# Performance work log

Measured on AMD Instinct MI355X. Metric: run time of the kernel, lower is better.

The kernel has to match this reference:

```python
import jax, jax.numpy as jnp
import numpy as np

H, C = 3, 64          # heads, out_channels
NEG_SLOPE = 0.2       # PyG GATConv leaky_relu default
LN_EPS = 1e-5


def setup_inputs() -> dict:
    key = jax.random.key(0)
    ks = jax.random.split(key, 20)
    N, E, D_in, edge_dim = 50000, 800000, 64, 5
    g = lambda k, shape: (jax.random.normal(k, shape, dtype=jnp.float32) * 0.1)
    return {
        "x": jax.random.normal(ks[0], (N, D_in), dtype=jnp.float32),
        "edge_attr": jax.random.normal(ks[1], (E, edge_dim), dtype=jnp.float32),
        "lin_w": g(ks[2], (D_in, H * C)),          # GATConv.lin (bias=False)
        "att_src": g(ks[3], (H, C)),
        "att_dst": g(ks[4], (H, C)),
        "lin_edge_w": g(ks[5], (edge_dim, H * C)),  # GATConv.lin_edge (bias=False)
        "att_edge": g(ks[6], (H, C)),
        "gat_bias": jnp.zeros((H * C,), jnp.float32),
        "w1": g(ks[7], (H * C, C)),
        "b1": jnp.zeros((C,), jnp.float32),
        "ln1_g": jnp.ones((C,), jnp.float32),
        "ln1_b": jnp.zeros((C,), jnp.float32),
        "w2": g(ks[8], (C, C)),
        "b2": jnp.zeros((C,), jnp.float32),
        "ln2_g": jnp.ones((C,), jnp.float32),
        "ln2_b": jnp.zeros((C,), jnp.float32),
        "edge_index": jax.random.randint(ks[9], (2, E), 0, N),
    }


def layer_norm(x, g, b):
    m = jnp.mean(x, axis=-1, keepdims=True)
    v = jnp.mean((x - m) ** 2, axis=-1, keepdims=True)
    return (x - m) * jax.lax.rsqrt(v + LN_EPS) * g + b


def gat_conv(x, edge_index, edge_attr, lin_w, att_src, att_dst,
             lin_edge_w, att_edge, gat_bias):
    N = x.shape[0]
    src, dst = edge_index[0], edge_index[1]

    # add_self_loops=True with fill_value='mean': self-loop edge_attr is the
    # per-node mean of incoming edge attributes (0 if node has no in-edges).
    attr_sum = jax.ops.segment_sum(edge_attr, dst, num_segments=N)       # [N, edge_dim]
    cnt = jax.ops.segment_sum(jnp.ones((dst.shape[0],), edge_attr.dtype), dst, num_segments=N)
    loop_attr = attr_sum / jnp.maximum(cnt, 1.0)[:, None]
    loop = jnp.arange(N, dtype=src.dtype)
    src = jnp.concatenate([src, loop])
    dst = jnp.concatenate([dst, loop])
    ea = jnp.concatenate([edge_attr, loop_attr], axis=0)                  # [E2, edge_dim]

    xs = (x @ lin_w).reshape(N, H, C)                                     # [N, H, C]
    a_src = jnp.einsum('nhc,hc->nh', xs, att_src)                         # [N, H]
    a_dst = jnp.einsum('nhc,hc->nh', xs, att_dst)                         # [N, H]
    e = (ea @ lin_edge_w).reshape(-1, H, C)                               # [E2, H, C]
    a_edge = jnp.einsum('ehc,hc->eh', e, att_edge)                        # [E2, H]

    logits = a_src[src] + a_dst[dst] + a_edge                             # [E2, H]
    logits = jnp.where(logits >= 0, logits, NEG_SLOPE * logits)           # leaky_relu

    # segment softmax over incoming edges of each dst node (self loops ensure non-empty)
    lmax = jax.ops.segment_max(logits, dst, num_segments=N)               # [N, H]
    ex = jnp.exp(logits - lmax[dst])
    denom = jax.ops.segment_sum(ex, dst, num_segments=N)                  # [N, H]
    alpha = ex / denom[dst]                                               # [E2, H]

    msgs = alpha[:, :, None] * xs[src]                                    # [E2, H, C]
    out = jax.ops.segment_sum(msgs, dst, num_segments=N)                  # [N, H, C]
    return out.reshape(N, H * C) + gat_bias


def reference(x, edge_attr, lin_w, att_src, att_dst, lin_edge_w, att_edge,
              gat_bias, w1, b1, ln1_g, ln1_b, w2, b2, ln2_g, ln2_b, edge_index):
    x_gat = gat_conv(x, edge_index, edge_attr, lin_w, att_src, att_dst,
                     lin_edge_w, att_edge, gat_bias)
    x_gat = x_gat @ w1 + b1                         # linear1: [N, C]
    x_gat = layer_norm(x + x_gat, ln1_g, ln1_b)     # layerNorm1(x + x_gat)
    lin = x_gat @ w2 + b2                           # linear2
    out = layer_norm(lin + x_gat, ln2_g, ln2_b)     # layerNorm2(lin + x_gat)
    return out                                      # dropout p=0 -> identity
```

## Files before the change

### kernel.cpp

```cpp
#include <hip/hip_runtime.h>


#define HH 3
#define CC 64
#define DIN 64
#define ED 5
#define HC 192
#define NEG_SLOPE 0.2f
#define LN_EPS 1e-5f
#define LOG2E 1.44269504f

typedef __attribute__((ext_vector_type(8))) short bf16x8;
typedef __attribute__((ext_vector_type(4))) float f32x4;

__device__ __forceinline__ float leaky(float l) { return fmaxf(l, NEG_SLOPE * l); }

__device__ __forceinline__ unsigned short f2bf(float f) {
    unsigned u = __float_as_uint(f);
    unsigned r = (u + 0x7FFFu + ((u >> 16) & 1u)) >> 16;
    return (unsigned short)r;
}
__device__ __forceinline__ float bf2f(unsigned short u) {
    return __uint_as_float((unsigned)u << 16);
}
__device__ __forceinline__ float bf_lo(unsigned v) { return __uint_as_float(v << 16); }
__device__ __forceinline__ float bf_hi(unsigned v) { return __uint_as_float(v & 0xFFFF0000u); }
__device__ __forceinline__ float rdl_f(float v, int i) {
    return __int_as_float(__builtin_amdgcn_readlane(__float_as_int(v), i));
}

__device__ __forceinline__ bf16x8 pack8(float4 a, float4 b) {
    bf16x8 r;
    r[0] = (short)f2bf(a.x); r[1] = (short)f2bf(a.y);
    r[2] = (short)f2bf(a.z); r[3] = (short)f2bf(a.w);
    r[4] = (short)f2bf(b.x); r[5] = (short)f2bf(b.y);
    r[6] = (short)f2bf(b.z); r[7] = (short)f2bf(b.w);
    return r;
}

#define PREP_TOT (HC*DIN + DIN*HC + CC*CC + CC + ED*HH)
#define PREP_BLOCKS 30
__global__ __launch_bounds__(256) void k_prep_cnt(const float* __restrict__ lin_w,
                                                  const float* __restrict__ w1,
                                                  const float* __restrict__ w2,
                                                  const float* __restrict__ b1,
                                                  const float* __restrict__ gat_bias,
                                                  const float* __restrict__ lin_edge_w,
                                                  const float* __restrict__ att_edge,
                                                  unsigned short* __restrict__ linwt,
                                                  unsigned short* __restrict__ w1t,
                                                  unsigned short* __restrict__ w2t,
                                                  float* __restrict__ b1p,
                                                  float* __restrict__ we,
                                                  const int* __restrict__ ei,
                                                  int* __restrict__ icnt, int E) {
    if (blockIdx.x < PREP_BLOCKS) {
        for (int i = blockIdx.x * 256 + threadIdx.x; i < PREP_TOT; i += PREP_BLOCKS * 256) {
            if (i < HC * DIN) {
                int c = i >> 6, k = i & 63;
                linwt[i] = f2bf(lin_w[k * HC + c]);
            } else if (i < 2 * HC * DIN) {
                int j = i - HC * DIN;
                int c = j / HC, k = j - c * HC;
                w1t[j] = f2bf(w1[k * CC + c]);
            } else if (i < 2 * HC * DIN + CC * CC) {
                int j = i - 2 * HC * DIN;
                int c = j >> 6, k = j & 63;
                w2t[j] = f2bf(w2[k * CC + c]);
            } else if (i < 2 * HC * DIN + CC * CC + CC) {
                int c = i - (2 * HC * DIN + CC * CC);
                float s = b1[c];
                for (int k = 0; k < HC; ++k) s += gat_bias[k] * w1[k * CC + c];
                b1p[c] = s;
            } else {
                int q = i - (2 * HC * DIN + CC * CC + CC);
                int d = q / HH, h = q - d * HH;
                float s = 0.f;
                for (int c = 0; c < CC; ++c)
                    s += lin_edge_w[d * HC + h * CC + c] * att_edge[h * CC + c];
                we[q] = s * LOG2E;
            }
        }
    } else {
        int nb = gridDim.x - PREP_BLOCKS;
        for (int e = (blockIdx.x - PREP_BLOCKS) * 256 + threadIdx.x; e < E; e += nb * 256)
            atomicAdd(&icnt[ei[E + e]], 1);
    }
}

__global__ __launch_bounds__(256) void k_xs(const float* __restrict__ x,
                                            const unsigned short* __restrict__ linwt,
                                            const float* __restrict__ att_src,
                                            const float* __restrict__ att_dst,
                                            unsigned short* __restrict__ xsb,
                                            float* __restrict__ a_src,
                                            float* __restrict__ a_dst, int N) {
    int lane = threadIdx.x & 63, w = threadIdx.x >> 6;
    int l15 = lane & 15, kg = (lane >> 4) * 8;
    int nb = blockIdx.x * 64;
    int arow = nb + w * 16 + l15;
    int arow_c = min(arow, N - 1);

    f32x4 acc[12];
    #pragma unroll
    for (int ct = 0; ct < 12; ++ct) acc[ct] = (f32x4){0.f, 0.f, 0.f, 0.f};

    #pragma unroll
    for (int k0 = 0; k0 < DIN; k0 += 32) {
        const float* ap = x + (size_t)arow_c * DIN + k0 + kg;
        float4 a0 = *(const float4*)ap;
        float4 a1 = *(const float4*)(ap + 4);
        bf16x8 af = pack8(a0, a1);
        #pragma unroll
        for (int ct = 0; ct < 12; ++ct) {
            bf16x8 bf = *(const bf16x8*)(linwt + (size_t)(ct * 16 + l15) * DIN + k0 + kg);
            acc[ct] = __builtin_amdgcn_mfma_f32_16x16x32_bf16(af, bf, acc[ct], 0, 0, 0);
        }
    }

    float asv[12], adv[12];
    #pragma unroll
    for (int ct = 0; ct < 12; ++ct) {
        int c = ct * 16 + l15;
        asv[ct] = att_src[c]; adv[ct] = att_dst[c];
    }

    int rbase = nb + w * 16 + (lane >> 4) * 4;
    #pragma unroll
    for (int j = 0; j < 4; ++j) {
        int r = rbase + j;
        bool ok = r < N;
        float ps0 = 0.f, ps1 = 0.f, ps2 = 0.f, pd0 = 0.f, pd1 = 0.f, pd2 = 0.f;
        #pragma unroll
        for (int ct = 0; ct < 12; ++ct) {
            float v = acc[ct][j];
            float s = v * asv[ct], d = v * adv[ct];
            if (ct < 4)      { ps0 += s; pd0 += d; }
            else if (ct < 8) { ps1 += s; pd1 += d; }
            else             { ps2 += s; pd2 += d; }
        }
        if (ok) {
            unsigned* row32 = (unsigned*)(xsb + (size_t)r * HC);
            #pragma unroll
            for (int ct = 0; ct < 4; ++ct) {
                int c = ct * 16 + l15;
                row32[c] = (unsigned)f2bf(acc[ct][j]) | ((unsigned)f2bf(acc[ct + 4][j]) << 16);
                xsb[(size_t)r * HC + 128 + c] = f2bf(acc[ct + 8][j]);
            }
        }
        #pragma unroll
        for (int o = 1; o < 16; o <<= 1) {
            ps0 += __shfl_xor(ps0, o, 64); pd0 += __shfl_xor(pd0, o, 64);
            ps1 += __shfl_xor(ps1, o, 64); pd1 += __shfl_xor(pd1, o, 64);
            ps2 += __shfl_xor(ps2, o, 64); pd2 += __shfl_xor(pd2, o, 64);
        }
        if (ok && l15 == 0) {
            a_src[r * HH + 0] = ps0 * LOG2E; a_src[r * HH + 1] = ps1 * LOG2E;
            a_src[r * HH + 2] = ps2 * LOG2E;
            a_dst[r * HH + 0] = pd0 * LOG2E; a_dst[r * HH + 1] = pd1 * LOG2E;
            a_dst[r * HH + 2] = pd2 * LOG2E;
        }
    }
}

__global__ __launch_bounds__(256) void k_scanA(const int* __restrict__ icnt,
                                               int* __restrict__ gtot,
                                               int* __restrict__ off,
                                               int* __restrict__ cursor, int N) {
    int i = blockIdx.x * 256 + threadIdx.x;
    int lane = threadIdx.x & 63, wid = threadIdx.x >> 6;
    int v = (i < N) ? icnt[i] : 0;
    int incl = v;
    #pragma unroll
    for (int o = 1; o < 64; o <<= 1) {
        int u = __shfl_up(incl, o, 64);
        if (lane >= o) incl += u;
    }
    __shared__ int wt[4];
    __shared__ int base_sh;
    if (lane == 63) wt[wid] = incl;
    __syncthreads();
    if (threadIdx.x == 0)
        base_sh = atomicAdd(gtot, wt[0] + wt[1] + wt[2] + wt[3]);
    __syncthreads();
    int wpre = 0;
    for (int w = 0; w < wid; ++w) wpre += wt[w];
    int excl = base_sh + wpre + incl - v;
    if (i < N) {
        off[i] = excl;
        cursor[i] = excl;
    }
}

__global__ __launch_bounds__(256) void k_fill(const float* __restrict__ ea,
                                              const int* __restrict__ ei,
                                              const float* __restrict__ a_src,
                                              const float* __restrict__ a_dst,
                                              const float* __restrict__ we,
                                              int* __restrict__ cursor,
                                              uint4* __restrict__ payload, int E) {
    int e = blockIdx.x * blockDim.x + threadIdx.x;
    if (e >= E) return;
    int s = ei[e], d = ei[E + e];
    float attr[ED];
    #pragma unroll
    for (int j = 0; j < ED; ++j) attr[j] = ea[(size_t)e * ED + j];
    float aeh[HH], lp[HH];
    #pragma unroll
    for (int h = 0; h < HH; ++h) {
        float a = 0.f;
        #pragma unroll
        for (int j = 0; j < ED; ++j) a += attr[j] * we[j * HH + h];
        aeh[h] = a;
        lp[h] = a_src[s * HH + h] + a_dst[d * HH + h] + a;
    }
    int pos = atomicAdd(&cursor[d], 1);
    uint4 pk;
    pk.x = (unsigned)f2bf(lp[0])  | ((unsigned)f2bf(lp[1])  << 16);
    pk.y = (unsigned)f2bf(lp[2])  | ((unsigned)f2bf(aeh[0]) << 16);
    pk.z = (unsigned)f2bf(aeh[1]) | ((unsigned)f2bf(aeh[2]) << 16);
    pk.w = (unsigned)s;
    payload[pos] = pk;
}

__global__ __launch_bounds__(256) void k_gat(const unsigned short* __restrict__ xsb,
                                             const float* __restrict__ a_src,
                                             const float* __restrict__ a_dst,
                                             const int* __restrict__ off,
                                             const int* __restrict__ icnt,
                                             const uint4* __restrict__ payload,
                                             unsigned short* __restrict__ oaccb, int N) {
    int lane = threadIdx.x & 63;
    int wid  = threadIdx.x >> 6;
    const unsigned* xs32 = (const unsigned*)xsb;
    unsigned c128ml = 128u - (unsigned)lane;
    for (int n = blockIdx.x * 4 + wid; n < N; n += gridDim.x * 4) {
        int beg = off[n];
        int deg = icnt[n];

        float pden0 = 0.f, pden1 = 0.f, pden2 = 0.f;
        float pae0 = 0.f, pae1 = 0.f, pae2 = 0.f;
        float a0A = 0.f, a1A = 0.f, a2A = 0.f;
        float a0B = 0.f, a1B = 0.f, a2B = 0.f;

        for (int c0 = 0; c0 < deg; c0 += 64) {
            int cn = min(deg - c0, 64);
            float w0 = 0.f, w1 = 0.f, w2 = 0.f;
            int srcv = 0;
            if (lane < cn) {
                uint4 p = payload[beg + c0 + lane];
                w0 = exp2f(leaky(bf_lo(p.x)));
                w1 = exp2f(leaky(bf_hi(p.x)));
                w2 = exp2f(leaky(bf_lo(p.y)));
                pae0 += bf_hi(p.y);
                pae1 += bf_lo(p.z);
                pae2 += bf_hi(p.z);
                pden0 += w0; pden1 += w1; pden2 += w2;
                srcv = (int)p.w;
            }
            int i = 0;
            for (; i + 2 <= cn; i += 2) {
                float ta0 = rdl_f(w0, i),     ta1 = rdl_f(w1, i),     ta2 = rdl_f(w2, i);
                int   sa  = __builtin_amdgcn_readlane(srcv, i);
                float tb0 = rdl_f(w0, i + 1), tb1 = rdl_f(w1, i + 1), tb2 = rdl_f(w2, i + 1);
                int   sb  = __builtin_amdgcn_readlane(srcv, i + 1);
                unsigned ia = (unsigned)sa * 96u + lane;
                unsigned ib = (unsigned)sb * 96u + lane;
                unsigned va = xs32[ia];
                unsigned vb = xs32[ib];
                float xa2 = bf2f(xsb[(ia << 1) + c128ml]);
                float xb2 = bf2f(xsb[(ib << 1) + c128ml]);
                a0A += ta0 * bf_lo(va); a1A += ta1 * bf_hi(va); a2A += ta2 * xa2;
                a0B += tb0 * bf_lo(vb); a1B += tb1 * bf_hi(vb); a2B += tb2 * xb2;
            }
            if (i < cn) {
                float ta0 = rdl_f(w0, i), ta1 = rdl_f(w1, i), ta2 = rdl_f(w2, i);
                int   sa  = __builtin_amdgcn_readlane(srcv, i);
                unsigned ia = (unsigned)sa * 96u + lane;
                unsigned va = xs32[ia];
                a0A += ta0 * bf_lo(va);
                a1A += ta1 * bf_hi(va);
                a2A += ta2 * bf2f(xsb[(ia << 1) + c128ml]);
            }
        }

        #pragma unroll
        for (int o = 32; o; o >>= 1) {
            pden0 += __shfl_xor(pden0, o, 64);
            pden1 += __shfl_xor(pden1, o, 64);
            pden2 += __shfl_xor(pden2, o, 64);
            pae0  += __shfl_xor(pae0, o, 64);
            pae1  += __shfl_xor(pae1, o, 64);
            pae2  += __shfl_xor(pae2, o, 64);
        }

        float dc = fmaxf((float)deg, 1.0f);
        float inv_dc = __builtin_amdgcn_rcpf(dc);
        float sl0 = leaky(a_src[n * HH + 0] + a_dst[n * HH + 0] + pae0 * inv_dc);
        float sl1 = leaky(a_src[n * HH + 1] + a_dst[n * HH + 1] + pae1 * inv_dc);
        float sl2 = leaky(a_src[n * HH + 2] + a_dst[n * HH + 2] + pae2 * inv_dc);
        float e0 = exp2f(sl0), e1 = exp2f(sl1), e2 = exp2f(sl2);
        unsigned ian = (unsigned)n * 96u + lane;
        unsigned van = xs32[ian];
        float xn2 = bf2f(xsb[(ian << 1) + c128ml]);
        float r0 = __builtin_amdgcn_rcpf(pden0 + e0);
        float r1 = __builtin_amdgcn_rcpf(pden1 + e1);
        float r2 = __builtin_amdgcn_rcpf(pden2 + e2);
        float acc0 = (a0A + a0B + e0 * bf_lo(van)) * r0;
        float acc1 = (a1A + a1B + e1 * bf_hi(van)) * r1;
        float acc2 = (a2A + a2B + e2 * xn2) * r2;
        size_t nbse = (size_t)n * HC;
        oaccb[nbse + 0 * CC + lane] = f2bf(acc0);
        oaccb[nbse + 1 * CC + lane] = f2bf(acc1);
        oaccb[nbse + 2 * CC + lane] = f2bf(acc2);
    }
}

__global__ __launch_bounds__(256) void k_mlp(const unsigned short* __restrict__ oaccb,
                                             const unsigned short* __restrict__ w1t,
                                             const unsigned short* __restrict__ w2t,
                                             const float* __restrict__ b1p,
                                             const float* __restrict__ x,
                                             const float* __restrict__ g1,
                                             const float* __restrict__ be1,
                                             const float* __restrict__ b2,
                                             const float* __restrict__ g2,
                                             const float* __restrict__ be2,
                                             float* __restrict__ out, int N) {
    __shared__ unsigned short H1[64 * 72];
    int lane = threadIdx.x & 63, w = threadIdx.x >> 6;
    int l15 = lane & 15, kg = (lane >> 4) * 8;
    int nb = blockIdx.x * 64;
    int arow = nb + w * 16 + l15;
    int arow_c = min(arow, N - 1);

    float c_b1[4], c_g1[4], c_be1[4], c_b2[4], c_g2[4], c_be2[4];
    #pragma unroll
    for (int ct = 0; ct < 4; ++ct) {
        int c = ct * 16 + l15;
        c_b1[ct] = b1p[c]; c_g1[ct] = g1[c]; c_be1[ct] = be1[c];
        c_b2[ct] = b2[c];  c_g2[ct] = g2[c]; c_be2[ct] = be2[c];
    }

    f32x4 acc[4];
    #pragma unroll
    for (int ct = 0; ct < 4; ++ct) acc[ct] = (f32x4){0.f, 0.f, 0.f, 0.f};
    #pragma unroll
    for (int k0 = 0; k0 < HC; k0 += 32) {
        bf16x8 af = *(const bf16x8*)(oaccb + (size_t)arow_c * HC + k0 + kg);
        #pragma unroll
        for (int ct = 0; ct < 4; ++ct) {
            bf16x8 bf = *(const bf16x8*)(w1t + (size_t)(ct * 16 + l15) * HC + k0 + kg);
            acc[ct] = __builtin_amdgcn_mfma_f32_16x16x32_bf16(af, bf, acc[ct], 0, 0, 0);
        }
    }

    int rbase = nb + w * 16 + (lane >> 4) * 4;
    int rloc0 = w * 16 + (lane >> 4) * 4;
    float h1v[4][4];
    float y[4][4];
    #pragma unroll
    for (int j = 0; j < 4; ++j) {
        int r = min(rbase + j, N - 1);
        #pragma unroll
        for (int ct = 0; ct < 4; ++ct)
            y[ct][j] = acc[ct][j] + c_b1[ct] + x[(size_t)r * DIN + ct * 16 + l15];
    }
    #pragma unroll
    for (int j = 0; j < 4; ++j) {
        float s = y[0][j] + y[1][j] + y[2][j] + y[3][j];
        #pragma unroll
        for (int o = 1; o < 16; o <<= 1) s += __shfl_xor(s, o, 64);
        float m = s * (1.0f / CC);
        float vs = 0.f;
        #pragma unroll
        for (int ct = 0; ct < 4; ++ct) { float d = y[ct][j] - m; vs += d * d; }
        #pragma unroll
        for (int o = 1; o < 16; o <<= 1) vs += __shfl_xor(vs, o, 64);
        float inv = rsqrtf(vs * (1.0f / CC) + LN_EPS);
        #pragma unroll
        for (int ct = 0; ct < 4; ++ct) {
            float h = (y[ct][j] - m) * inv * c_g1[ct] + c_be1[ct];
            h1v[ct][j] = h;
            H1[(rloc0 + j) * 72 + ct * 16 + l15] = f2bf(h);
        }
    }
    __syncthreads();

    f32x4 acc2[4];
    #pragma unroll
    for (int ct = 0; ct < 4; ++ct) acc2[ct] = (f32x4){0.f, 0.f, 0.f, 0.f};
    #pragma unroll
    for (int k0 = 0; k0 < CC; k0 += 32) {
        bf16x8 af = *(const bf16x8*)&H1[(w * 16 + l15) * 72 + k0 + kg];
        #pragma unroll
        for (int ct = 0; ct < 4; ++ct) {
            bf16x8 bf = *(const bf16x8*)(w2t + (size_t)(ct * 16 + l15) * CC + k0 + kg);
            acc2[ct] = __builtin_amdgcn_mfma_f32_16x16x32_bf16(af, bf, acc2[ct], 0, 0, 0);
        }
    }

    #pragma unroll
    for (int j = 0; j < 4; ++j) {
        float z0 = acc2[0][j] + c_b2[0] + h1v[0][j];
        float z1 = acc2[1][j] + c_b2[1] + h1v[1][j];
        float z2 = acc2[2][j] + c_b2[2] + h1v[2][j];
        float z3 = acc2[3][j] + c_b2[3] + h1v[3][j];
        float s = z0 + z1 + z2 + z3;
        #pragma unroll
        for (int o = 1; o < 16; o <<= 1) s += __shfl_xor(s, o, 64);
        float m = s * (1.0f / CC);
        float d0 = z0 - m, d1 = z1 - m, d2 = z2 - m, d3 = z3 - m;
        float vs = d0 * d0 + d1 * d1 + d2 * d2 + d3 * d3;
        #pragma unroll
        for (int o = 1; o < 16; o <<= 1) vs += __shfl_xor(vs, o, 64);
        float inv = rsqrtf(vs * (1.0f / CC) + LN_EPS);
        int r = rbase + j;
        if (r < N) {
            out[(size_t)r * CC + 0 * 16 + l15] = d0 * inv * c_g2[0] + c_be2[0];
            out[(size_t)r * CC + 1 * 16 + l15] = d1 * inv * c_g2[1] + c_be2[1];
            out[(size_t)r * CC + 2 * 16 + l15] = d2 * inv * c_g2[2] + c_be2[2];
            out[(size_t)r * CC + 3 * 16 + l15] = d3 * inv * c_g2[3] + c_be2[3];
        }
    }
}

extern "C" void kernel_launch(void* const* d_in, const int* in_sizes, int n_in,
                              void* d_out, int out_size, void* d_ws, size_t ws_size,
                              hipStream_t stream) {
    const float* x          = (const float*)d_in[0];
    const float* edge_attr  = (const float*)d_in[1];
    const float* lin_w      = (const float*)d_in[2];
    const float* att_src    = (const float*)d_in[3];
    const float* att_dst    = (const float*)d_in[4];
    const float* lin_edge_w = (const float*)d_in[5];
    const float* att_edge   = (const float*)d_in[6];
    const float* gat_bias   = (const float*)d_in[7];
    const float* w1         = (const float*)d_in[8];
    const float* b1         = (const float*)d_in[9];
    const float* ln1_g      = (const float*)d_in[10];
    const float* ln1_b      = (const float*)d_in[11];
    const float* w2         = (const float*)d_in[12];
    const float* b2         = (const float*)d_in[13];
    const float* ln2_g      = (const float*)d_in[14];
    const float* ln2_b      = (const float*)d_in[15];
    const int*   ei         = (const int*)d_in[16];
    float* out = (float*)d_out;

    const int N = in_sizes[0] / DIN;
    const int E = in_sizes[1] / ED;
    const int nb_scan = (N + 255) / 256;

    char* ws = (char*)d_ws;
    size_t off_b = 0;
    auto alloc = [&](size_t bytes) {
        size_t o = off_b;
        off_b = (off_b + bytes + 255) & ~(size_t)255;
        return o;
    };
    int* icnt = (int*)(ws + alloc((size_t)N * 4));
    int* gtot = (int*)(ws + alloc(4));
    size_t zero_bytes = off_b;
    unsigned short* xsb   = (unsigned short*)(ws + alloc((size_t)N * HC * 2));
    unsigned short* oaccb = (unsigned short*)(ws + alloc((size_t)N * HC * 2));
    float*  a_srcb  = (float*)(ws + alloc((size_t)N * HH * 4));
    float*  a_dstb  = (float*)(ws + alloc((size_t)N * HH * 4));
    int*    offb    = (int*)(ws + alloc((size_t)N * 4));
    int*    cursor  = (int*)(ws + alloc((size_t)N * 4));
    uint4*  payload = (uint4*)(ws + alloc((size_t)E * 16));
    unsigned short* linwt = (unsigned short*)(ws + alloc((size_t)HC * DIN * 2));
    unsigned short* w1t   = (unsigned short*)(ws + alloc((size_t)DIN * HC * 2));
    unsigned short* w2t   = (unsigned short*)(ws + alloc((size_t)CC * CC * 2));
    float* b1p = (float*)(ws + alloc((size_t)CC * 4));
    float* we  = (float*)(ws + alloc((size_t)ED * HH * 4));
    (void)ws_size; (void)n_in; (void)out_size;

    hipMemsetAsync(d_ws, 0, zero_bytes, stream);

    k_prep_cnt<<<PREP_BLOCKS + (E + 255) / 256, 256, 0, stream>>>(
        lin_w, w1, w2, b1, gat_bias, lin_edge_w, att_edge,
        linwt, w1t, w2t, b1p, we, ei, icnt, E);
    k_xs<<<(N + 63) / 64, 256, 0, stream>>>(x, linwt, att_src, att_dst, xsb, a_srcb, a_dstb, N);
    k_scanA<<<nb_scan, 256, 0, stream>>>(icnt, gtot, offb, cursor, N);
    k_fill<<<(E + 255) / 256, 256, 0, stream>>>(edge_attr, ei, a_srcb, a_dstb, we, cursor,
                                                payload, E);
    k_gat<<<(N + 3) / 4, 256, 0, stream>>>(xsb, a_srcb, a_dstb, offb, icnt, payload, oaccb, N);
    k_mlp<<<(N + 63) / 64, 256, 0, stream>>>(oaccb, w1t, w2t, b1p, x,
                                             ln1_g, ln1_b, b2, ln2_g, ln2_b, out, N);
}
```

Baseline: 186.9 us.

## Merge scan into xs kernel, stage edge weights in LDS, hoist fill atomic

The block-level scan of in-degree counts now runs as extra blocks of the xs projection kernel, which removes one kernel launch. In the gather kernel, per-edge weights and source indices are written to a per-wave LDS buffer and read back as float4 instead of being broadcast with readlane. The fill kernel issues its cursor atomic earlier so its latency can overlap the attribute loads, and the index multiplies use __umul24. These are several unrelated tweaks, and the LDS staging adds shared-memory traffic where readlane had none.

New measurement: 184.9 us. Within noise of the previous version (-1.0%).

```diff
diff --git a/kernel.cpp b/kernel.cpp
--- a/kernel.cpp
+++ b/kernel.cpp
@@ -25,9 +25,6 @@
 }
 __device__ __forceinline__ float bf_lo(unsigned v) { return __uint_as_float(v << 16); }
 __device__ __forceinline__ float bf_hi(unsigned v) { return __uint_as_float(v & 0xFFFF0000u); }
-__device__ __forceinline__ float rdl_f(float v, int i) {
-    return __int_as_float(__builtin_amdgcn_readlane(__float_as_int(v), i));
-}
 
 __device__ __forceinline__ bf16x8 pack8(float4 a, float4 b) {
     bf16x8 r;
@@ -94,7 +91,37 @@
                                             const float* __restrict__ att_dst,
                                             unsigned short* __restrict__ xsb,
                                             float* __restrict__ a_src,
-                                            float* __restrict__ a_dst, int N) {
+                                            float* __restrict__ a_dst,
+                                            const int* __restrict__ icnt,
+                                            int* __restrict__ gtot,
+                                            int* __restrict__ off,
+                                            int* __restrict__ cursor,
+                                            int N, int nbx) {
+    __shared__ int wt[4];
+    __shared__ int base_sh;
+    if ((int)blockIdx.x >= nbx) {
+        int bid = blockIdx.x - nbx;
+        int i = bid * 256 + threadIdx.x;
+        int lane = threadIdx.x & 63, wid = threadIdx.x >> 6;
+        int v = (i < N) ? icnt[i] : 0;
+        int incl = v;
+        #pragma unroll
+        for (int o = 1; o < 64; o <<= 1) {
+            int u = __shfl_up(incl, o, 64);
+            if (lane >= o) incl += u;
+        }
+        if (lane == 63) wt[wid] = incl;
+        __syncthreads();
+        if (threadIdx.x == 0)
+            base_sh = atomicAdd(gtot, wt[0] + wt[1] + wt[2] + wt[3]);
+        __syncthreads();
+        int wpre = 0;
+        for (int w2 = 0; w2 < wid; ++w2) wpre += wt[w2];
+        int excl = base_sh + wpre + incl - v;
+        if (i < N) { off[i] = excl; cursor[i] = excl; }
+        return;
+    }
+
     int lane = threadIdx.x & 63, w = threadIdx.x >> 6;
     int l15 = lane & 15, kg = (lane >> 4) * 8;
     int nb = blockIdx.x * 64;
@@ -160,35 +187,6 @@
             a_dst[r * HH + 0] = pd0 * LOG2E; a_dst[r * HH + 1] = pd1 * LOG2E;
             a_dst[r * HH + 2] = pd2 * LOG2E;
         }
-    }
-}
-
-__global__ __launch_bounds__(256) void k_scanA(const int* __restrict__ icnt,
-                                               int* __restrict__ gtot,
-                                               int* __restrict__ off,
-                                               int* __restrict__ cursor, int N) {
-    int i = blockIdx.x * 256 + threadIdx.x;
-    int lane = threadIdx.x & 63, wid = threadIdx.x >> 6;
-    int v = (i < N) ? icnt[i] : 0;
-    int incl = v;
-    #pragma unroll
-    for (int o = 1; o < 64; o <<= 1) {
-        int u = __shfl_up(incl, o, 64);
-        if (lane >= o) incl += u;
-    }
-    __shared__ int wt[4];
-    __shared__ int base_sh;
-    if (lane == 63) wt[wid] = incl;
-    __syncthreads();
-    if (threadIdx.x == 0)
-        base_sh = atomicAdd(gtot, wt[0] + wt[1] + wt[2] + wt[3]);
-    __syncthreads();
-    int wpre = 0;
-    for (int w = 0; w < wid; ++w) wpre += wt[w];
-    int excl = base_sh + wpre + incl - v;
-    if (i < N) {
-        off[i] = excl;
-        cursor[i] = excl;
     }
 }
 
@@ -202,6 +200,7 @@
     int e = blockIdx.x * blockDim.x + threadIdx.x;
     if (e >= E) return;
     int s = ei[e], d = ei[E + e];
+    int pos = atomicAdd(&cursor[d], 1);
     float attr[ED];
     #pragma unroll
     for (int j = 0; j < ED; ++j) attr[j] = ea[(size_t)e * ED + j];
@@ -214,7 +213,6 @@
         aeh[h] = a;
         lp[h] = a_src[s * HH + h] + a_dst[d * HH + h] + a;
     }
-    int pos = atomicAdd(&cursor[d], 1);
     uint4 pk;
     pk.x = (unsigned)f2bf(lp[0])  | ((unsigned)f2bf(lp[1])  << 16);
     pk.y = (unsigned)f2bf(lp[2])  | ((unsigned)f2bf(aeh[0]) << 16);
@@ -230,6 +228,7 @@
                                              const int* __restrict__ icnt,
                                              const uint4* __restrict__ payload,
                                              unsigned short* __restrict__ oaccb, int N) {
+    __shared__ float4 wbuf[4][64];
     int lane = threadIdx.x & 63;
     int wid  = threadIdx.x >> 6;
     const unsigned* xs32 = (const unsigned*)xsb;
@@ -246,7 +245,7 @@
         for (int c0 = 0; c0 < deg; c0 += 64) {
             int cn = min(deg - c0, 64);
             float w0 = 0.f, w1 = 0.f, w2 = 0.f;
-            int srcv = 0;
+            int src = 0;
             if (lane < cn) {
                 uint4 p = payload[beg + c0 + lane];
                 w0 = exp2f(leaky(bf_lo(p.x)));
@@ -256,31 +255,29 @@
                 pae1 += bf_lo(p.z);
                 pae2 += bf_hi(p.z);
                 pden0 += w0; pden1 += w1; pden2 += w2;
-                srcv = (int)p.w;
+                src = (int)p.w;
             }
+            wbuf[wid][lane] = make_float4(w0, w1, w2, __int_as_float(src));
             int i = 0;
             for (; i + 2 <= cn; i += 2) {
-                float ta0 = rdl_f(w0, i),     ta1 = rdl_f(w1, i),     ta2 = rdl_f(w2, i);
-                int   sa  = __builtin_amdgcn_readlane(srcv, i);
-                float tb0 = rdl_f(w0, i + 1), tb1 = rdl_f(w1, i + 1), tb2 = rdl_f(w2, i + 1);
-                int   sb  = __builtin_amdgcn_readlane(srcv, i + 1);
-                unsigned ia = (unsigned)sa * 96u + lane;
-                unsigned ib = (unsigned)sb * 96u + lane;
+                float4 ta = wbuf[wid][i];
+                float4 tb = wbuf[wid][i + 1];
+                unsigned ia = __umul24((unsigned)__float_as_int(ta.w), 96u) + lane;
+                unsigned ib = __umul24((unsigned)__float_as_int(tb.w), 96u) + lane;
                 unsigned va = xs32[ia];
                 unsigned vb = xs32[ib];
                 float xa2 = bf2f(xsb[(ia << 1) + c128ml]);
                 float xb2 = bf2f(xsb[(ib << 1) + c128ml]);
-                a0A += ta0 * bf_lo(va); a1A += ta1 * bf_hi(va); a2A += ta2 * xa2;
-                a0B += tb0 * bf_lo(vb); a1B += tb1 * bf_hi(vb); a2B += tb2 * xb2;
+                a0A += ta.x * bf_lo(va); a1A += ta.y * bf_hi(va); a2A += ta.z * xa2;
+                a0B += tb.x * bf_lo(vb); a1B += tb.y * bf_hi(vb); a2B += tb.z * xb2;
             }
             if (i < cn) {
-                float ta0 = rdl_f(w0, i), ta1 = rdl_f(w1, i), ta2 = rdl_f(w2, i);
-                int   sa  = __builtin_amdgcn_readlane(srcv, i);
-                unsigned ia = (unsigned)sa * 96u + lane;
+                float4 ta = wbuf[wid][i];
+                unsigned ia = __umul24((unsigned)__float_as_int(ta.w), 96u) + lane;
                 unsigned va = xs32[ia];
-                a0A += ta0 * bf_lo(va);
-                a1A += ta1 * bf_hi(va);
-                a2A += ta2 * bf2f(xsb[(ia << 1) + c128ml]);
+                a0A += ta.x * bf_lo(va);
+                a1A += ta.y * bf_hi(va);
+                a2A += ta.z * bf2f(xsb[(ia << 1) + c128ml]);
             }
         }
 
@@ -300,7 +297,7 @@
         float sl1 = leaky(a_src[n * HH + 1] + a_dst[n * HH + 1] + pae1 * inv_dc);
         float sl2 = leaky(a_src[n * HH + 2] + a_dst[n * HH + 2] + pae2 * inv_dc);
         float e0 = exp2f(sl0), e1 = exp2f(sl1), e2 = exp2f(sl2);
-        unsigned ian = (unsigned)n * 96u + lane;
+        unsigned ian = __umul24((unsigned)n, 96u) + lane;
         unsigned van = xs32[ian];
         float xn2 = bf2f(xsb[(ian << 1) + c128ml]);
         float r0 = __builtin_amdgcn_rcpf(pden0 + e0);
@@ -450,6 +447,7 @@
     const int N = in_sizes[0] / DIN;
     const int E = in_sizes[1] / ED;
     const int nb_scan = (N + 255) / 256;
+    const int nbx = (N + 63) / 64;
 
     char* ws = (char*)d_ws;
     size_t off_b = 0;
@@ -480,8 +478,9 @@
     k_prep_cnt<<<PREP_BLOCKS + (E + 255) / 256, 256, 0, stream>>>(
         lin_w, w1, w2, b1, gat_bias, lin_edge_w, att_edge,
         linwt, w1t, w2t, b1p, we, ei, icnt, E);
-    k_xs<<<(N + 63) / 64, 256, 0, stream>>>(x, linwt, att_src, att_dst, xsb, a_srcb, a_dstb, N);
-    k_scanA<<<nb_scan, 256, 0, stream>>>(icnt, gtot, offb, cursor, N);
+    k_xs<<<nbx + nb_scan, 256, 0, stream>>>(x, linwt, att_src, att_dst, xsb,
+                                            a_srcb, a_dstb, icnt, gtot, offb, cursor,
+                                            N, nbx);
     k_fill<<<(E + 255) / 256, 256, 0, stream>>>(edge_attr, ei, a_srcb, a_dstb, we, cursor,
                                                 payload, E);
     k_gat<<<(N + 3) / 4, 256, 0, stream>>>(xsb, a_srcb, a_dstb, offb, icnt, payload, oaccb, N);
```
